# Kernel optimization log

Hardware: AMD Instinct MI355X
Metric: run time of the kernel (lower is better)

## Reference

```python
import jax, jax.numpy as jnp
import numpy as np

N = 50000
E = 800000
IN_DIM = 512
H1 = IN_DIM // 2   # 256
H2 = IN_DIM // 4   # 128
D = 8
NP_CAYLEY = D * (D - 1) // 2  # 28


def setup_inputs() -> dict:
    key = jax.random.key(0)
    ks = jax.random.split(key, 10)
    x = jax.random.normal(ks[0], (N, IN_DIM), dtype=jnp.float32)
    edge_index = jax.random.randint(ks[1], (2, E), 0, N, dtype=jnp.int64)
    s1 = 1.0 / np.sqrt(IN_DIM)
    s2 = 1.0 / np.sqrt(H1)
    s3 = 1.0 / np.sqrt(H2)
    W1l = jax.random.uniform(ks[2], (H1, IN_DIM), jnp.float32, -s1, s1)
    b1 = jax.random.uniform(ks[3], (H1,), jnp.float32, -s1, s1)
    W1r = jax.random.uniform(ks[4], (H1, IN_DIM), jnp.float32, -s1, s1)
    W2l = jax.random.uniform(ks[5], (H2, H1), jnp.float32, -s2, s2)
    b2 = jax.random.uniform(ks[6], (H2,), jnp.float32, -s2, s2)
    W2r = jax.random.uniform(ks[7], (H2, H1), jnp.float32, -s2, s2)
    Wp = jax.random.uniform(ks[8], (NP_CAYLEY, H2), jnp.float32, -s3, s3)
    bp = jax.random.uniform(ks[9], (NP_CAYLEY,), jnp.float32, -s3, s3)
    return {"x": x, "edge_index": edge_index,
            "W1l": W1l, "b1": b1, "W1r": W1r,
            "W2l": W2l, "b2": b2, "W2r": W2r,
            "Wp": Wp, "bp": bp}


def _sage_conv(x, src, dst, Wl, bl, Wr):
    # PyG SAGEConv (mean aggr): out = lin_l(mean_{j in N(i)} x_j) + lin_r(x_i)
    msg_sum = jax.ops.segment_sum(x[src], dst, num_segments=N)  # [N, F]
    deg = jax.ops.segment_sum(jnp.ones((src.shape[0],), x.dtype), dst,
                              num_segments=N)
    mean = msg_sum / jnp.maximum(deg, 1.0)[:, None]
    return mean @ Wl.T + bl + x @ Wr.T


def _cayley(params):
    # params: [N, d(d-1)/2] -> skew A, then O = (I - A)^{-1} (I + A)
    iu, ju = jnp.triu_indices(D, k=1)  # row-major i<j matches torch loop order
    n = params.shape[0]
    A = jnp.zeros((n, D, D), params.dtype)
    A = A.at[:, iu, ju].set(params)
    A = A.at[:, ju, iu].set(-params)
    I = jnp.eye(D, dtype=params.dtype)
    return jnp.linalg.solve(I[None] - A, I[None] + A)


def reference(x, edge_index, W1l, b1, W1r, W2l, b2, W2r, Wp, bp):
    src, dst = edge_index[0], edge_index[1]
    h = jax.nn.relu(_sage_conv(x, src, dst, W1l, b1, W1r))
    h = jax.nn.relu(_sage_conv(h, src, dst, W2l, b2, W2r))
    params = h @ Wp.T + bp  # [N, 28]
    return _cayley(params)  # [N, 8, 8]
```

## Files before the change

### kernel.cpp

```cpp
#include <hip/hip_runtime.h>
#include <hip/hip_bf16.h>


#define WS_ALIGN(x) (((x) + 255) & ~size_t(255))

typedef __attribute__((ext_vector_type(8))) short short8;
typedef __attribute__((ext_vector_type(4))) float floatx4;

static __device__ __forceinline__ ushort f2b(float f) {
    unsigned u = __builtin_bit_cast(unsigned, f);
    u = (u + 0x7fffu + ((u >> 16) & 1u)) >> 16;
    return (ushort)u;
}
static __device__ __forceinline__ float b2f(ushort h) {
    unsigned u = ((unsigned)h) << 16;
    return __builtin_bit_cast(float, u);
}
static __device__ __forceinline__ unsigned pk2(float a, float b) {
    return (unsigned)f2b(a) | ((unsigned)f2b(b) << 16);
}


__global__ __launch_bounds__(256)
void prep_kernel(const float* __restrict__ W1l, const float* __restrict__ W1r,
                 const float* __restrict__ W2l, const float* __restrict__ W2r,
                 ushort* __restrict__ Wc1, ushort* __restrict__ Wc2) {
    int idx = blockIdx.x * blockDim.x + threadIdx.x;
    const int n1 = (512 * 512) / 8;
    const int n2 = (256 * 256) / 8;
    const float* src;
    ushort* dstp;
    if (idx < n1) {
        int e = idx * 8;
        int row = e >> 9, col = e & 511;
        src = (row < 256) ? &W1l[row * 512 + col] : &W1r[(row - 256) * 512 + col];
        dstp = &Wc1[e];
    } else if (idx < n1 + n2) {
        int e = (idx - n1) * 8;
        int row = e >> 8, col = e & 255;
        src = (row < 128) ? &W2l[row * 256 + col] : &W2r[(row - 128) * 256 + col];
        dstp = &Wc2[e];
    } else {
        return;
    }
    const float4* s4 = reinterpret_cast<const float4*>(src);
    float4 v0 = s4[0], v1 = s4[1];
    short8 o;
    o[0] = (short)f2b(v0.x); o[1] = (short)f2b(v0.y);
    o[2] = (short)f2b(v0.z); o[3] = (short)f2b(v0.w);
    o[4] = (short)f2b(v1.x); o[5] = (short)f2b(v1.y);
    o[6] = (short)f2b(v1.z); o[7] = (short)f2b(v1.w);
    *reinterpret_cast<short8*>(dstp) = o;
}


__global__ __launch_bounds__(256)
void scan_phase1(const int* __restrict__ deg, int* __restrict__ bsum, int n) {
    __shared__ int red[256];
    const int t = threadIdx.x;
    const int i = blockIdx.x * 1024 + t * 4;
    int s = 0;
    if (i + 4 <= n) {
        int4 v = *reinterpret_cast<const int4*>(&deg[i]);
        s = v.x + v.y + v.z + v.w;
    } else {
        for (int k = i; k < n; ++k) s += deg[k];
    }
    red[t] = s;
    __syncthreads();
#pragma unroll
    for (int off = 128; off > 0; off >>= 1) {
        if (t < off) red[t] += red[t + off];
        __syncthreads();
    }
    if (t == 0) bsum[blockIdx.x] = red[0];
}

__global__ __launch_bounds__(256)
void scan_phase2(int* __restrict__ bsum, int* __restrict__ rowptr, int nb, int n) {
    __shared__ int sh[256];
    const int t = threadIdx.x;
    int orig = (t < nb) ? bsum[t] : 0;
    sh[t] = orig;
    __syncthreads();
#pragma unroll
    for (int off = 1; off < 256; off <<= 1) {
        int v = (t >= off) ? sh[t - off] : 0;
        __syncthreads();
        sh[t] += v;
        __syncthreads();
    }
    if (t < nb) bsum[t] = sh[t] - orig;
    if (t == 255) rowptr[n] = sh[255];
}

__global__ __launch_bounds__(256)
void scan_phase3(const int* __restrict__ deg, const int* __restrict__ bsum,
                 int* __restrict__ rowptr, int* __restrict__ cursor, int n) {
    __shared__ int red[256];
    const int t = threadIdx.x;
    const int i = blockIdx.x * 1024 + t * 4;
    int v0 = 0, v1 = 0, v2 = 0, v3 = 0;
    if (i + 4 <= n) {
        int4 v = *reinterpret_cast<const int4*>(&deg[i]);
        v0 = v.x; v1 = v.y; v2 = v.z; v3 = v.w;
    } else {
        if (i     < n) v0 = deg[i];
        if (i + 1 < n) v1 = deg[i + 1];
        if (i + 2 < n) v2 = deg[i + 2];
        if (i + 3 < n) v3 = deg[i + 3];
    }
    int s = v0 + v1 + v2 + v3;
    red[t] = s;
    __syncthreads();
#pragma unroll
    for (int off = 1; off < 256; off <<= 1) {
        int u = (t >= off) ? red[t - off] : 0;
        __syncthreads();
        red[t] += u;
        __syncthreads();
    }
    int pre = bsum[blockIdx.x] + red[t] - s;
    if (i + 4 <= n) {
        int4 o;
        o.x = pre; o.y = pre + v0; o.z = pre + v0 + v1; o.w = pre + v0 + v1 + v2;
        *reinterpret_cast<int4*>(&rowptr[i]) = o;
        *reinterpret_cast<int4*>(&cursor[i]) = make_int4(0, 0, 0, 0);
    } else {
        if (i     < n) { rowptr[i]     = pre;                cursor[i]     = 0; }
        if (i + 1 < n) { rowptr[i + 1] = pre + v0;           cursor[i + 1] = 0; }
        if (i + 2 < n) { rowptr[i + 2] = pre + v0 + v1;      cursor[i + 2] = 0; }
        if (i + 3 < n) { rowptr[i + 3] = pre + v0 + v1 + v2; cursor[i + 3] = 0; }
    }
}

__global__ void scatter_kernel(const int* __restrict__ src, const int* __restrict__ dst,
                               const int* __restrict__ rowptr, int* __restrict__ cursor,
                               int* __restrict__ adj, int E) {
    int e = blockIdx.x * blockDim.x + threadIdx.x;
    if (e < E) {
        int d = dst[e];
        int p = atomicAdd(&cursor[d], 1);
        adj[rowptr[d] + p] = src[e];
    }
}


template <bool CASTA, int BN, bool HIST>
__global__ __launch_bounds__(512, 4)
void gemm_wide(const float* __restrict__ Af, const ushort* __restrict__ Ab,
               const ushort* __restrict__ B,
               ushort* __restrict__ Cl, ushort* __restrict__ Cr,
               int M, int K, int S, int gmy,
               const int* __restrict__ hdst, int* __restrict__ hdeg, int hE) {
    if (HIST) {
        if (blockIdx.y >= gmy) {
            int e = ((blockIdx.y - gmy) * gridDim.x + blockIdx.x) * 512 + threadIdx.x;
            if (e < hE) atomicAdd(&hdeg[hdst[e]], 1);
            return;
        }
    }
    constexpr int WN = BN / 4;
    constexpr int NI = BN / 64;
    __shared__ ushort As[128 * 64];
    __shared__ ushort Bs[BN * 64];
    const int tid  = threadIdx.x;
    const int wave = tid >> 6;
    const int lane = tid & 63;
    const int row0 = blockIdx.y * 128;
    const int col0 = blockIdx.x * BN;
    const int wm = (wave & 1) * 64;
    const int wn = (wave >> 1) * WN;

    floatx4 acc[4][NI];
#pragma unroll
    for (int i = 0; i < 4; ++i)
#pragma unroll
        for (int j = 0; j < NI; ++j)
            acc[i][j] = (floatx4){0.f, 0.f, 0.f, 0.f};

    const int rsub = lane >> 3;
    const int ksw  = ((lane & 7) * 16) ^ (rsub << 4);

    const int ar = tid >> 2;
    const int aq = tid & 3;
    int agrow = row0 + ar; if (agrow >= M) agrow = M - 1;
    const float* arow_base = CASTA ? (Af + (size_t)agrow * K + aq * 16) : nullptr;
    char* alds = (char*)As + ar * 128;
    const int arx = (ar & 7) << 4;

    float4 va0, va1, va2, va3;
    if constexpr (CASTA) {
        const float* s0 = arow_base;
        va0 = *reinterpret_cast<const float4*>(s0 + 0);
        va1 = *reinterpret_cast<const float4*>(s0 + 4);
        va2 = *reinterpret_cast<const float4*>(s0 + 8);
        va3 = *reinterpret_cast<const float4*>(s0 + 12);
    }

    for (int k0 = 0; k0 < K; k0 += 64) {
#pragma unroll
        for (int i = 0; i < NI; ++i) {
            int chunk = wave * NI + i;
            int r = chunk * 8 + rsub;
            int gcol = col0 + r;
            const char* src = (const char*)(B + (size_t)gcol * K + k0) + ksw;
            __builtin_amdgcn_global_load_lds(
                (const __attribute__((address_space(1))) unsigned int*)src,
                (__attribute__((address_space(3))) unsigned int*)(&Bs[chunk * 512]),
                16, 0, 0);
        }
        if constexpr (CASTA) {
            uint4 o0 = make_uint4(pk2(va0.x, va0.y), pk2(va0.z, va0.w),
                                  pk2(va1.x, va1.y), pk2(va1.z, va1.w));
            uint4 o1 = make_uint4(pk2(va2.x, va2.y), pk2(va2.z, va2.w),
                                  pk2(va3.x, va3.y), pk2(va3.z, va3.w));
            int g0 = aq * 2;
            *reinterpret_cast<uint4*>(alds + ((g0 * 16) ^ arx))       = o0;
            *reinterpret_cast<uint4*>(alds + (((g0 + 1) * 16) ^ arx)) = o1;
            if (k0 + 64 < K) {
                const float* s1 = arow_base + k0 + 64;
                va0 = *reinterpret_cast<const float4*>(s1 + 0);
                va1 = *reinterpret_cast<const float4*>(s1 + 4);
                va2 = *reinterpret_cast<const float4*>(s1 + 8);
                va3 = *reinterpret_cast<const float4*>(s1 + 12);
            }
        } else {
#pragma unroll
            for (int i = 0; i < 2; ++i) {
                int chunk = wave * 2 + i;
                int r = chunk * 8 + rsub;
                int grow = row0 + r;
                if (grow >= M) grow = M - 1;
                const char* src = (const char*)(Ab + (size_t)grow * K + k0) + ksw;
                __builtin_amdgcn_global_load_lds(
                    (const __attribute__((address_space(1))) unsigned int*)src,
                    (__attribute__((address_space(3))) unsigned int*)(&As[chunk * 512]),
                    16, 0, 0);
            }
        }
        __syncthreads();

#pragma unroll
        for (int kk = 0; kk < 2; ++kk) {
            short8 af[4], bf[NI];
            const int kb = (kk * 64 + ((lane >> 4) << 4)) ^ ((lane & 7) << 4);
#pragma unroll
            for (int im = 0; im < 4; ++im) {
                int r = wm + im * 16 + (lane & 15);
                af[im] = *reinterpret_cast<const short8*>((const char*)As + r * 128 + kb);
            }
#pragma unroll
            for (int in = 0; in < NI; ++in) {
                int r = wn + in * 16 + (lane & 15);
                bf[in] = *reinterpret_cast<const short8*>((const char*)Bs + r * 128 + kb);
            }
#pragma unroll
            for (int im = 0; im < 4; ++im)
#pragma unroll
                for (int in = 0; in < NI; ++in)
                    acc[im][in] = __builtin_amdgcn_mfma_f32_16x16x32_bf16(
                        af[im], bf[in], acc[im][in], 0, 0, 0);
        }
        __syncthreads();
    }

#pragma unroll
    for (int im = 0; im < 4; ++im) {
#pragma unroll
        for (int reg = 0; reg < 4; ++reg) {
            int r = row0 + wm + im * 16 + ((lane >> 4) << 2) + reg;
            if (r < M) {
#pragma unroll
                for (int in = 0; in < NI; ++in) {
                    int g = col0 + wn + in * 16 + (lane & 15);
                    if (g < S) Cl[(size_t)r * S + g] = f2b(acc[im][in][reg]);
                    else       Cr[(size_t)r * S + (g - S)] = f2b(acc[im][in][reg]);
                }
            }
        }
    }
}


template <int LPN>
__global__ __launch_bounds__(256)
void aggregate_bf16(const ushort* __restrict__ Yl, const ushort* __restrict__ Yr,
                    const float* __restrict__ bias,
                    const int* __restrict__ rowptr, const int* __restrict__ adj,
                    ushort* __restrict__ H, int n) {
    constexpr int F = LPN * 8;
    const int grp = threadIdx.x / LPN;
    const int sub = threadIdx.x % LPN;
    const int node = blockIdx.x * (256 / LPN) + grp;
    if (node >= n) return;
    const int c = sub * 8;
    const int start = rowptr[node], end = rowptr[node + 1];

    float acc[8];
#pragma unroll
    for (int v = 0; v < 8; ++v) acc[v] = 0.f;

    int e = start;
    for (; e + 4 <= end; e += 4) {
        int s0 = adj[e + 0], s1 = adj[e + 1], s2 = adj[e + 2], s3 = adj[e + 3];
        short8 r0 = *reinterpret_cast<const short8*>(&Yl[(size_t)s0 * F + c]);
        short8 r1 = *reinterpret_cast<const short8*>(&Yl[(size_t)s1 * F + c]);
        short8 r2 = *reinterpret_cast<const short8*>(&Yl[(size_t)s2 * F + c]);
        short8 r3 = *reinterpret_cast<const short8*>(&Yl[(size_t)s3 * F + c]);
#pragma unroll
        for (int v = 0; v < 8; ++v)
            acc[v] += (b2f((ushort)r0[v]) + b2f((ushort)r1[v])) +
                      (b2f((ushort)r2[v]) + b2f((ushort)r3[v]));
    }
    for (; e < end; ++e) {
        int s = adj[e];
        short8 r = *reinterpret_cast<const short8*>(&Yl[(size_t)s * F + c]);
#pragma unroll
        for (int v = 0; v < 8; ++v) acc[v] += b2f((ushort)r[v]);
    }

    const int d = end - start;
    const float inv = 1.0f / (float)(d > 0 ? d : 1);
    short8 sv = *reinterpret_cast<const short8*>(&Yr[(size_t)node * F + c]);
    float4 bv0 = *reinterpret_cast<const float4*>(&bias[c]);
    float4 bv1 = *reinterpret_cast<const float4*>(&bias[c + 4]);
    float bb[8] = {bv0.x, bv0.y, bv0.z, bv0.w, bv1.x, bv1.y, bv1.z, bv1.w};
    short8 o;
#pragma unroll
    for (int v = 0; v < 8; ++v)
        o[v] = (short)f2b(fmaxf(acc[v] * inv + b2f((ushort)sv[v]) + bb[v], 0.f));
    *reinterpret_cast<short8*>(&H[(size_t)node * F + c]) = o;
}


__global__ __launch_bounds__(256)
void params_cayley(const ushort* __restrict__ H2, const float* __restrict__ Wp,
                   const float* __restrict__ bp, float* __restrict__ Out, int n) {
    __shared__ float WpS[32 * 132];
    __shared__ float bpS[32];
    __shared__ float Pl[32][36];
    for (int t = threadIdx.x; t < 32 * 132; t += 256) WpS[t] = 0.f;
    if (threadIdx.x < 32) bpS[threadIdx.x] = (threadIdx.x < 28) ? bp[threadIdx.x] : 0.f;
    __syncthreads();
    for (int t = threadIdx.x; t < 28 * 128; t += 256) {
        int r = t >> 7, c = t & 127;
        WpS[r * 132 + c] = Wp[t];
    }
    __syncthreads();

    const int g = threadIdx.x >> 3;
    const int l = threadIdx.x & 7;
    const int node = blockIdx.x * 32 + g;
    if (node < n) {
        short8 h8[16];
        const short8* hp = reinterpret_cast<const short8*>(&H2[(size_t)node * 128]);
#pragma unroll
        for (int q = 0; q < 16; ++q) h8[q] = hp[q];

        float acc0 = bpS[l], acc1 = bpS[l + 8], acc2 = bpS[l + 16], acc3 = bpS[l + 24];
#pragma unroll
        for (int q = 0; q < 32; ++q) {
            float h0 = b2f((ushort)h8[q >> 1][(q & 1) * 4 + 0]);
            float h1 = b2f((ushort)h8[q >> 1][(q & 1) * 4 + 1]);
            float h2 = b2f((ushort)h8[q >> 1][(q & 1) * 4 + 2]);
            float h3 = b2f((ushort)h8[q >> 1][(q & 1) * 4 + 3]);
            float4 w0 = *reinterpret_cast<const float4*>(&WpS[(l +  0) * 132 + 4 * q]);
            float4 w1 = *reinterpret_cast<const float4*>(&WpS[(l +  8) * 132 + 4 * q]);
            float4 w2 = *reinterpret_cast<const float4*>(&WpS[(l + 16) * 132 + 4 * q]);
            float4 w3 = *reinterpret_cast<const float4*>(&WpS[(l + 24) * 132 + 4 * q]);
            acc0 += h0 * w0.x + h1 * w0.y + h2 * w0.z + h3 * w0.w;
            acc1 += h0 * w1.x + h1 * w1.y + h2 * w1.z + h3 * w1.w;
            acc2 += h0 * w2.x + h1 * w2.y + h2 * w2.z + h3 * w2.w;
            acc3 += h0 * w3.x + h1 * w3.y + h2 * w3.z + h3 * w3.w;
        }
        Pl[g][l]      = acc0;
        Pl[g][l + 8]  = acc1;
        Pl[g][l + 16] = acc2;
        Pl[g][l + 24] = acc3;
    }
    __syncthreads();

    const int t = threadIdx.x;
    if (t < 32) {
        int nd = blockIdx.x * 32 + t;
        if (nd < n) {
            float p[28];
#pragma unroll
            for (int j = 0; j < 28; ++j) p[j] = Pl[t][j];

            float M_[8][8], B_[8][8];
#pragma unroll
            for (int r = 0; r < 8; ++r)
#pragma unroll
                for (int c = 0; c < 8; ++c) {
                    M_[r][c] = (r == c) ? 1.f : 0.f;
                    B_[r][c] = (r == c) ? 1.f : 0.f;
                }
            {
                int idx = 0;
#pragma unroll
                for (int r = 0; r < 8; ++r)
#pragma unroll
                    for (int c = r + 1; c < 8; ++c) {
                        float a = p[idx++];
                        M_[r][c] -= a;  M_[c][r] += a;
                        B_[r][c] += a;  B_[c][r] -= a;
                    }
            }
#pragma unroll
            for (int col = 0; col < 8; ++col) {
                float inv = 1.0f / M_[col][col];
#pragma unroll
                for (int c = 0; c < 8; ++c) { M_[col][c] *= inv; B_[col][c] *= inv; }
#pragma unroll
                for (int r = 0; r < 8; ++r) {
                    if (r == col) continue;
                    float f = M_[r][col];
#pragma unroll
                    for (int c = 0; c < 8; ++c) {
                        M_[r][c] -= f * M_[col][c];
                        B_[r][c] -= f * B_[col][c];
                    }
                }
            }
            float* out = &Out[(size_t)nd * 64];
#pragma unroll
            for (int r = 0; r < 8; ++r) {
                float4 o0 = make_float4(B_[r][0], B_[r][1], B_[r][2], B_[r][3]);
                float4 o1 = make_float4(B_[r][4], B_[r][5], B_[r][6], B_[r][7]);
                *reinterpret_cast<float4*>(&out[r * 8 + 0]) = o0;
                *reinterpret_cast<float4*>(&out[r * 8 + 4]) = o1;
            }
        }
    }
}


extern "C" void kernel_launch(void* const* d_in, const int* in_sizes, int n_in,
                              void* d_out, int out_size, void* d_ws, size_t ws_size,
                              hipStream_t stream) {
    const float* x   = (const float*)d_in[0];
    const int*   ei  = (const int*)d_in[1];
    const float* W1l = (const float*)d_in[2];
    const float* b1  = (const float*)d_in[3];
    const float* W1r = (const float*)d_in[4];
    const float* W2l = (const float*)d_in[5];
    const float* b2  = (const float*)d_in[6];
    const float* W2r = (const float*)d_in[7];
    const float* Wp  = (const float*)d_in[8];
    const float* bp  = (const float*)d_in[9];
    float* out = (float*)d_out;

    const int IN_DIM = 512;
    const int N = in_sizes[0] / IN_DIM;
    const int E = in_sizes[1] / 2;

    char* ws = (char*)d_ws;
    size_t off = 0;
    int* deg      = (int*)(ws + off); off = WS_ALIGN(off + (size_t)N * 4);
    int* rowptr   = (int*)(ws + off); off = WS_ALIGN(off + (size_t)(N + 1) * 4);
    int* cursor   = (int*)(ws + off); off = WS_ALIGN(off + (size_t)N * 4);
    int* bsum     = (int*)(ws + off); off = WS_ALIGN(off + (size_t)256 * 4);
    int* adj      = (int*)(ws + off); off = WS_ALIGN(off + (size_t)E * 4);
    ushort* Yl    = (ushort*)(ws + off); off = WS_ALIGN(off + (size_t)N * 256 * 2);
    ushort* Yr    = (ushort*)(ws + off); off = WS_ALIGN(off + (size_t)N * 256 * 2);
    ushort* h1    = (ushort*)(ws + off); off = WS_ALIGN(off + (size_t)N * 256 * 2);
    ushort* zl    = (ushort*)(ws + off); off = WS_ALIGN(off + (size_t)N * 128 * 2);
    ushort* zr    = (ushort*)(ws + off); off = WS_ALIGN(off + (size_t)N * 128 * 2);
    ushort* Wc1   = (ushort*)(ws + off); off = WS_ALIGN(off + (size_t)512 * 512 * 2);
    ushort* Wc2   = (ushort*)(ws + off); off = WS_ALIGN(off + (size_t)256 * 256 * 2);

    const int* src = ei;
    const int* dst = ei + E;

    hipMemsetAsync(deg, 0, (size_t)N * 4, stream);

    const int eb = (E + 255) / 256;
    const int wb = ((512 * 512 + 256 * 256) / 8 + 255) / 256;
    const int nb = (N + 1023) / 1024;
    const int gm = (N + 127) / 128;
    const int hb = (E + 1023) / 1024;

    prep_kernel<<<wb, 256, 0, stream>>>(W1l, W1r, W2l, W2r, Wc1, Wc2);

    gemm_wide<true, 256, true><<<dim3(2, gm + hb), 512, 0, stream>>>(
        x, (const ushort*)nullptr, Wc1, Yl, Yr, N, 512, 256, gm, dst, deg, E);

    scan_phase1<<<nb, 256, 0, stream>>>(deg, bsum, N);
    scan_phase2<<<1, 256, 0, stream>>>(bsum, rowptr, nb, N);
    scan_phase3<<<nb, 256, 0, stream>>>(deg, bsum, rowptr, cursor, N);
    scatter_kernel<<<eb, 256, 0, stream>>>(src, dst, rowptr, cursor, adj, E);

    aggregate_bf16<32><<<(N + 7) / 8, 256, 0, stream>>>(Yl, Yr, b1, rowptr, adj, h1, N);

    gemm_wide<false, 128, false><<<dim3(2, gm), 512, 0, stream>>>(
        (const float*)nullptr, h1, Wc2, zl, zr, N, 256, 128, gm,
        (const int*)nullptr, (int*)nullptr, 0);

    ushort* h2 = Yl;
    aggregate_bf16<16><<<(N + 15) / 16, 256, 0, stream>>>(zl, zr, b2, rowptr, adj, h2, N);

    params_cayley<<<(N + 31) / 32, 256, 0, stream>>>(h2, Wp, bp, out, N);
}
```

Before: 264.5 us.

## Fuse CSR build and weight prep into one cooperative grid-synced kernel

Replaces the memset, weight cast, histogram, three scan kernels and scatter with one cooperative kernel of 1024 blocks that uses grid.sync between phases. The histogram that was previously folded into the first GEMM launch moves out of it, so the GEMM no longer carries extra blocks. The aim is to cut launch overhead and inter-kernel gaps in the small CSR-building steps. The cost is that the CSR build no longer overlaps the first GEMM, grid-wide barriers are added, and the scan runs on a single wave per block. A non-cooperative fallback is kept for when the cooperative launch fails.

```diff
diff --git a/kernel.cpp b/kernel.cpp
--- a/kernel.cpp
+++ b/kernel.cpp
@@ -1,5 +1,8 @@
 #include <hip/hip_runtime.h>
 #include <hip/hip_bf16.h>
+#include <hip/hip_cooperative_groups.h>
+
+namespace cg = cooperative_groups;
 
 
 #define WS_ALIGN(x) (((x) + 255) & ~size_t(255))
@@ -20,14 +23,11 @@
     return (unsigned)f2b(a) | ((unsigned)f2b(b) << 16);
 }
 
-
-__global__ __launch_bounds__(256)
-void prep_kernel(const float* __restrict__ W1l, const float* __restrict__ W1r,
-                 const float* __restrict__ W2l, const float* __restrict__ W2r,
-                 ushort* __restrict__ Wc1, ushort* __restrict__ Wc2) {
-    int idx = blockIdx.x * blockDim.x + threadIdx.x;
+static __device__ __forceinline__ void wcat_elem(
+    int idx, const float* __restrict__ W1l, const float* __restrict__ W1r,
+    const float* __restrict__ W2l, const float* __restrict__ W2r,
+    ushort* __restrict__ Wc1, ushort* __restrict__ Wc2) {
     const int n1 = (512 * 512) / 8;
-    const int n2 = (256 * 256) / 8;
     const float* src;
     ushort* dstp;
     if (idx < n1) {
@@ -35,13 +35,11 @@
         int row = e >> 9, col = e & 511;
         src = (row < 256) ? &W1l[row * 512 + col] : &W1r[(row - 256) * 512 + col];
         dstp = &Wc1[e];
-    } else if (idx < n1 + n2) {
+    } else {
         int e = (idx - n1) * 8;
         int row = e >> 8, col = e & 255;
         src = (row < 128) ? &W2l[row * 256 + col] : &W2r[(row - 128) * 256 + col];
         dstp = &Wc2[e];
-    } else {
-        return;
     }
     const float4* s4 = reinterpret_cast<const float4*>(src);
     float4 v0 = s4[0], v1 = s4[1];
@@ -53,6 +51,117 @@
     *reinterpret_cast<short8*>(dstp) = o;
 }
 
+
+#define COOP_GRID 1024
+
+__global__ __launch_bounds__(256)
+void csr_coop(const int* __restrict__ src, const int* __restrict__ dst, int E, int N,
+              int* __restrict__ deg, int* __restrict__ rowptr, int* __restrict__ cursor,
+              int* __restrict__ bsum, int* __restrict__ adj,
+              const float* __restrict__ W1l, const float* __restrict__ W1r,
+              const float* __restrict__ W2l, const float* __restrict__ W2r,
+              ushort* __restrict__ Wc1, ushort* __restrict__ Wc2) {
+    cg::grid_group grid = cg::this_grid();
+    const int gtid = blockIdx.x * 256 + threadIdx.x;
+    const int gsz  = COOP_GRID * 256;
+
+    for (int i = gtid; i < N; i += gsz) deg[i] = 0;
+    const int nw = (512 * 512 + 256 * 256) / 8;
+    for (int i = gtid; i < nw; i += gsz)
+        wcat_elem(i, W1l, W1r, W2l, W2r, Wc1, Wc2);
+    grid.sync();
+
+    for (int e = gtid; e < E; e += gsz) atomicAdd(&deg[dst[e]], 1);
+    grid.sync();
+
+    const int chunk = (N + COOP_GRID - 1) / COOP_GRID;
+    const int base  = blockIdx.x * chunk;
+    const int lane  = threadIdx.x & 63;
+    const int wid   = threadIdx.x >> 6;
+    if (wid == 0) {
+        int carry = 0;
+        for (int c0 = 0; c0 < chunk; c0 += 64) {
+            int li = c0 + lane;
+            int idx = base + li;
+            int v = (li < chunk && idx < N) ? deg[idx] : 0;
+#pragma unroll
+            for (int off = 1; off < 64; off <<= 1) {
+                int u = __shfl_up(v, off);
+                if (lane >= off) v += u;
+            }
+            carry += __shfl(v, 63);
+        }
+        if (lane == 0) bsum[blockIdx.x] = carry;
+    }
+    grid.sync();
+
+    if (blockIdx.x == 0) {
+        __shared__ int sh[256];
+        const int t = threadIdx.x;
+        constexpr int PER = COOP_GRID / 256;
+        int vloc0, vloc1, vloc2, vloc3;
+        vloc0 = bsum[t * PER + 0]; vloc1 = bsum[t * PER + 1];
+        vloc2 = bsum[t * PER + 2]; vloc3 = bsum[t * PER + 3];
+        int s = vloc0 + vloc1 + vloc2 + vloc3;
+        sh[t] = s;
+        __syncthreads();
+        for (int off = 1; off < 256; off <<= 1) {
+            int u = (t >= off) ? sh[t - off] : 0;
+            __syncthreads();
+            sh[t] += u;
+            __syncthreads();
+        }
+        int pre = (t > 0) ? sh[t - 1] : 0;
+        bsum[t * PER + 0] = pre;                     pre += vloc0;
+        bsum[t * PER + 1] = pre;                     pre += vloc1;
+        bsum[t * PER + 2] = pre;                     pre += vloc2;
+        bsum[t * PER + 3] = pre;
+        if (t == 255) rowptr[N] = sh[255];
+    }
+    grid.sync();
+
+    if (wid == 0) {
+        int boff = bsum[blockIdx.x];
+        for (int c0 = 0; c0 < chunk; c0 += 64) {
+            int li = c0 + lane;
+            int idx = base + li;
+            int v = (li < chunk && idx < N) ? deg[idx] : 0;
+            int inc = v;
+#pragma unroll
+            for (int off = 1; off < 64; off <<= 1) {
+                int u = __shfl_up(inc, off);
+                if (lane >= off) inc += u;
+            }
+            if (li < chunk && idx < N) {
+                rowptr[idx] = boff + inc - v;
+                cursor[idx] = 0;
+            }
+            boff += __shfl(inc, 63);
+        }
+    }
+    grid.sync();
+
+    for (int e = gtid; e < E; e += gsz) {
+        int d = dst[e];
+        int p = atomicAdd(&cursor[d], 1);
+        adj[rowptr[d] + p] = src[e];
+    }
+}
+
+
+__global__ __launch_bounds__(256)
+void prep_kernel(const float* __restrict__ W1l, const float* __restrict__ W1r,
+                 const float* __restrict__ W2l, const float* __restrict__ W2r,
+                 ushort* __restrict__ Wc1, ushort* __restrict__ Wc2) {
+    int idx = blockIdx.x * blockDim.x + threadIdx.x;
+    if (idx < (512 * 512 + 256 * 256) / 8)
+        wcat_elem(idx, W1l, W1r, W2l, W2r, Wc1, Wc2);
+}
+
+__global__ void hist_kernel(const int* __restrict__ dst, int* __restrict__ deg, int E) {
+    int e = blockIdx.x * blockDim.x + threadIdx.x;
+    if (e < E) atomicAdd(&deg[dst[e]], 1);
+}
 
 __global__ __launch_bounds__(256)
 void scan_phase1(const int* __restrict__ deg, int* __restrict__ bsum, int n) {
@@ -146,20 +255,12 @@
 }
 
 
-template <bool CASTA, int BN, bool HIST>
+template <bool CASTA, int BN>
 __global__ __launch_bounds__(512, 4)
 void gemm_wide(const float* __restrict__ Af, const ushort* __restrict__ Ab,
                const ushort* __restrict__ B,
                ushort* __restrict__ Cl, ushort* __restrict__ Cr,
-               int M, int K, int S, int gmy,
-               const int* __restrict__ hdst, int* __restrict__ hdeg, int hE) {
-    if (HIST) {
-        if (blockIdx.y >= gmy) {
-            int e = ((blockIdx.y - gmy) * gridDim.x + blockIdx.x) * 512 + threadIdx.x;
-            if (e < hE) atomicAdd(&hdeg[hdst[e]], 1);
-            return;
-        }
-    }
+               int M, int K, int S) {
     constexpr int WN = BN / 4;
     constexpr int NI = BN / 64;
     __shared__ ushort As[128 * 64];
@@ -461,7 +562,7 @@
     int* deg      = (int*)(ws + off); off = WS_ALIGN(off + (size_t)N * 4);
     int* rowptr   = (int*)(ws + off); off = WS_ALIGN(off + (size_t)(N + 1) * 4);
     int* cursor   = (int*)(ws + off); off = WS_ALIGN(off + (size_t)N * 4);
-    int* bsum     = (int*)(ws + off); off = WS_ALIGN(off + (size_t)256 * 4);
+    int* bsum     = (int*)(ws + off); off = WS_ALIGN(off + (size_t)COOP_GRID * 4);
     int* adj      = (int*)(ws + off); off = WS_ALIGN(off + (size_t)E * 4);
     ushort* Yl    = (ushort*)(ws + off); off = WS_ALIGN(off + (size_t)N * 256 * 2);
     ushort* Yr    = (ushort*)(ws + off); off = WS_ALIGN(off + (size_t)N * 256 * 2);
@@ -474,30 +575,37 @@
     const int* src = ei;
     const int* dst = ei + E;
 
-    hipMemsetAsync(deg, 0, (size_t)N * 4, stream);
-
-    const int eb = (E + 255) / 256;
-    const int wb = ((512 * 512 + 256 * 256) / 8 + 255) / 256;
-    const int nb = (N + 1023) / 1024;
+    {
+        int E_ = E, N_ = N;
+        void* args[] = {
+            (void*)&src, (void*)&dst, (void*)&E_, (void*)&N_,
+            (void*)&deg, (void*)&rowptr, (void*)&cursor, (void*)&bsum, (void*)&adj,
+            (void*)&W1l, (void*)&W1r, (void*)&W2l, (void*)&W2r,
+            (void*)&Wc1, (void*)&Wc2 };
+        hipError_t cerr = hipLaunchCooperativeKernel(
+            (const void*)csr_coop, dim3(COOP_GRID), dim3(256), args, 0, stream);
+        if (cerr != hipSuccess) {
+            const int eb = (E + 255) / 256;
+            const int wb = ((512 * 512 + 256 * 256) / 8 + 255) / 256;
+            const int nb = (N + 1023) / 1024;
+            hipMemsetAsync(deg, 0, (size_t)N * 4, stream);
+            prep_kernel<<<wb, 256, 0, stream>>>(W1l, W1r, W2l, W2r, Wc1, Wc2);
+            hist_kernel<<<eb, 256, 0, stream>>>(dst, deg, E);
+            scan_phase1<<<nb, 256, 0, stream>>>(deg, bsum, N);
+            scan_phase2<<<1, 256, 0, stream>>>(bsum, rowptr, nb, N);
+            scan_phase3<<<nb, 256, 0, stream>>>(deg, bsum, rowptr, cursor, N);
+            scatter_kernel<<<eb, 256, 0, stream>>>(src, dst, rowptr, cursor, adj, E);
+        }
+    }
+
     const int gm = (N + 127) / 128;
-    const int hb = (E + 1023) / 1024;
-
-    prep_kernel<<<wb, 256, 0, stream>>>(W1l, W1r, W2l, W2r, Wc1, Wc2);
-
-    gemm_wide<true, 256, true><<<dim3(2, gm + hb), 512, 0, stream>>>(
-        x, (const ushort*)nullptr, Wc1, Yl, Yr, N, 512, 256, gm, dst, deg, E);
-
-    scan_phase1<<<nb, 256, 0, stream>>>(deg, bsum, N);
-    scan_phase2<<<1, 256, 0, stream>>>(bsum, rowptr, nb, N);
-    scan_phase3<<<nb, 256, 0, stream>>>(deg, bsum, rowptr, cursor, N);
-    scatter_kernel<<<eb, 256, 0, stream>>>(src, dst, rowptr, cursor, adj, E);
-
+
+    gemm_wide<true, 256><<<dim3(2, gm), 512, 0, stream>>>(
+        x, (const ushort*)nullptr, Wc1, Yl, Yr, N, 512, 256);
     aggregate_bf16<32><<<(N + 7) / 8, 256, 0, stream>>>(Yl, Yr, b1, rowptr, adj, h1, N);
 
-    gemm_wide<false, 128, false><<<dim3(2, gm), 512, 0, stream>>>(
-        (const float*)nullptr, h1, Wc2, zl, zr, N, 256, 128, gm,
-        (const int*)nullptr, (int*)nullptr, 0);
-
+    gemm_wide<false, 128><<<dim3(2, gm), 512, 0, stream>>>(
+        (const float*)nullptr, h1, Wc2, zl, zr, N, 256, 128);
     ushort* h2 = Yl;
     aggregate_bf16<16><<<(N + 15) / 16, 256, 0, stream>>>(zl, zr, b2, rowptr, adj, h2, N);
 
```

New measurement: 819.1 us. 210% more time.
